# Optimization experiments

Measured on AMD Instinct MI355X. Metric: run time of the kernel, lower is better.

## Reference

```python
import jax, jax.numpy as jnp
import numpy as np

INPUT_DIM = 1024
OUTPUT_DIM = 1024


def setup_inputs() -> dict:
    key = jax.random.key(0)
    k1, k2, k3, k4 = jax.random.split(key, 4)
    B, S, D = 4, 2048, INPUT_DIM
    src = jax.random.normal(k1, (B, S, D), dtype=jnp.float32)
    tgt = jax.random.normal(k2, (B, S, D), dtype=jnp.float32)
    # nn.Linear(input_dim*2, output_dim): weight [out, in], bias [out]
    bound = 1.0 / np.sqrt(2 * D)
    W = jax.random.uniform(k3, (OUTPUT_DIM, 2 * D), jnp.float32, -bound, bound)
    b = jax.random.uniform(k4, (OUTPUT_DIM,), jnp.float32, -bound, bound)
    return {"src": src, "tgt": tgt, "W": W, "b": b}


def reference(src, tgt, W, b):
    # weight = bmm(tgt, src^T): [B, S_tgt, S_src]
    weight = jnp.einsum("btd,bsd->bts", tgt, src)
    # NOTE: original uses Softmax(dim=1) -> normalizes over the tgt axis
    weight = jax.nn.softmax(weight, axis=1)
    # weighted sum over src positions: [B, S_tgt, D]
    weight_sum = jnp.einsum("bts,bsd->btd", weight, src)
    output = jnp.concatenate([weight_sum, tgt], axis=2)  # [B, S_tgt, 2D]
    output = output @ W.T + b  # [B, S_tgt, output_dim]
    return (output, weight)
```

## Files before the change

kernel.cpp:

```cpp
#include <hip/hip_runtime.h>
#include <stdint.h>


#define B_   4
#define S_   2048
#define D_   1024
#define OUTD 1024

typedef unsigned short ushort_t;
typedef _Float16 half8 __attribute__((ext_vector_type(8)));
typedef float    f32x4 __attribute__((ext_vector_type(4)));

__device__ __forceinline__ ushort_t f2h(float f) {
    union { _Float16 h; ushort_t u; } v;
    v.h = (_Float16)f;
    return v.u;
}
__device__ __forceinline__ float h2f(ushort_t u) {
    union { _Float16 h; ushort_t u; } v;
    v.u = u;
    return (float)v.h;
}

__device__ __forceinline__ void ld16(const ushort_t* g, ushort_t* l) {
    __builtin_amdgcn_global_load_lds(
        (const __attribute__((address_space(1))) void*)g,
        (__attribute__((address_space(3))) void*)l, 16, 0, 0);
}


__global__ void k_split(const float4* __restrict__ src, const float4* __restrict__ tgt,
                        ushort4* __restrict__ sh,
                        ushort4* __restrict__ th, ushort4* __restrict__ tl)
{
    const int64_t n4 = (int64_t)B_ * S_ * D_ / 4;
    for (int64_t i = (int64_t)blockIdx.x * blockDim.x + threadIdx.x; i < n4;
         i += (int64_t)gridDim.x * blockDim.x) {
        float4 s = src[i];
        sh[i] = (ushort4){f2h(s.x), f2h(s.y), f2h(s.z), f2h(s.w)};
        float4 tv = tgt[i];
        ushort4 ht = {f2h(tv.x), f2h(tv.y), f2h(tv.z), f2h(tv.w)};
        th[i] = ht;
        tl[i] = (ushort4){f2h(tv.x - h2f(ht.x)), f2h(tv.y - h2f(ht.y)),
                          f2h(tv.z - h2f(ht.z)), f2h(tv.w - h2f(ht.w))};
    }
}

__global__ void k_wconv(const float4* __restrict__ W, ushort4* __restrict__ wb)
{
    const int64_t n4 = (int64_t)OUTD * 2 * D_ / 4;
    for (int64_t i = (int64_t)blockIdx.x * blockDim.x + threadIdx.x; i < n4;
         i += (int64_t)gridDim.x * blockDim.x) {
        float4 w = W[i];
        wb[i] = (ushort4){f2h(w.x), f2h(w.y), f2h(w.z), f2h(w.w)};
    }
}

__launch_bounds__(512, 2)
__global__ void k_gemm_logits(const ushort_t* __restrict__ Ah, const ushort_t* __restrict__ Al,
                              const ushort_t* __restrict__ Bs,
                              float* __restrict__ C,
                              float* __restrict__ pm, float* __restrict__ ps)
{
    const int M = S_, N = S_, K = D_;
    int b = blockIdx.z;
    Ah += (int64_t)b * M * K;  Al += (int64_t)b * M * K;
    Bs += (int64_t)b * N * K;
    C  += (int64_t)b * M * N;

    __shared__ __align__(16) ushort_t lds[2 * 24576];
    __shared__ float red_m[4][256], red_s[4][256];

    int t    = threadIdx.x;
    int m0   = blockIdx.y * 256, n0 = blockIdx.x * 256;
    int wave = t >> 6, lane = t & 63;
    int wr   = (wave >> 1) * 64;
    int wc   = (wave & 1) * 128;
    int l15  = lane & 15, quad = lane >> 4;

    f32x4 acc[4][8];
#pragma unroll
    for (int i = 0; i < 4; i++)
#pragma unroll
        for (int j = 0; j < 8; j++) acc[i][j] = (f32x4){0.f, 0.f, 0.f, 0.f};

    int pr   = t >> 3;
    int slot = t & 7;
    int cg   = slot ^ (pr & 7);
    int srow = pr * 2 + (cg >> 2);
    int scol = (cg & 3) * 8;

    const ushort_t* gAh = Ah + (int64_t)(m0 + srow) * K + scol;
    const ushort_t* gAl = Al + (int64_t)(m0 + srow) * K + scol;
    const ushort_t* gB  = Bs + (int64_t)(n0 + srow) * K + scol;
    const int64_t rstep = (int64_t)128 * K;

    auto stage = [&](int bufi, int kofs) {
        ushort_t* Lb = lds + bufi * 24576 + t * 8;
        ld16(gAh + kofs,         Lb);
        ld16(gAh + rstep + kofs, Lb + 4096);
        ld16(gAl + kofs,         Lb + 8192);
        ld16(gAl + rstep + kofs, Lb + 12288);
        ld16(gB  + kofs,         Lb + 16384);
        ld16(gB  + rstep + kofs, Lb + 20480);
    };

    int aoff[4], boff[8];
#pragma unroll
    for (int i = 0; i < 4; i++) {
        int R = wr + i * 16 + l15;
        int p = R >> 1, c = ((R & 1) << 2) + quad;
        aoff[i] = p * 64 + ((c ^ (p & 7)) << 3);
    }
#pragma unroll
    for (int j = 0; j < 8; j++) {
        int R = wc + j * 16 + l15;
        int p = R >> 1, c = ((R & 1) << 2) + quad;
        boff[j] = p * 64 + ((c ^ (p & 7)) << 3);
    }

    stage(0, 0);
    int buf = 0;

    for (int kt = 0; kt < 32; ++kt) {
        asm volatile("s_waitcnt vmcnt(0)" ::: "memory");
        __builtin_amdgcn_s_barrier();
        asm volatile("" ::: "memory");
        __builtin_amdgcn_sched_barrier(0);

        if (kt < 31) stage(buf ^ 1, (kt + 1) * 32);

        const ushort_t* Lb = lds + buf * 24576;
        half8 ah[4], al[4], bf[4];
#pragma unroll
        for (int i = 0; i < 4; i++) {
            ah[i] = *(const half8*)(Lb + aoff[i]);
            al[i] = *(const half8*)(Lb + 8192 + aoff[i]);
        }
#pragma unroll
        for (int j = 0; j < 4; j++) bf[j] = *(const half8*)(Lb + 16384 + boff[j]);

        __builtin_amdgcn_s_setprio(1);
#pragma unroll
        for (int i = 0; i < 4; i++)
#pragma unroll
            for (int j = 0; j < 4; j++)
                acc[i][j] = __builtin_amdgcn_mfma_f32_16x16x32_f16(ah[i], bf[j], acc[i][j], 0, 0, 0);
#pragma unroll
        for (int i = 0; i < 4; i++)
#pragma unroll
            for (int j = 0; j < 4; j++)
                acc[i][j] = __builtin_amdgcn_mfma_f32_16x16x32_f16(al[i], bf[j], acc[i][j], 0, 0, 0);
        __builtin_amdgcn_s_setprio(0);

#pragma unroll
        for (int j = 0; j < 4; j++) bf[j] = *(const half8*)(Lb + 16384 + boff[4 + j]);

        __builtin_amdgcn_s_setprio(1);
#pragma unroll
        for (int i = 0; i < 4; i++)
#pragma unroll
            for (int j = 0; j < 4; j++)
                acc[i][4 + j] = __builtin_amdgcn_mfma_f32_16x16x32_f16(ah[i], bf[j], acc[i][4 + j], 0, 0, 0);
#pragma unroll
        for (int i = 0; i < 4; i++)
#pragma unroll
            for (int j = 0; j < 4; j++)
                acc[i][4 + j] = __builtin_amdgcn_mfma_f32_16x16x32_f16(al[i], bf[j], acc[i][4 + j], 0, 0, 0);
        __builtin_amdgcn_s_setprio(0);

        buf ^= 1;
    }

#pragma unroll
    for (int i = 0; i < 4; i++) {
        int row_base = m0 + wr + i * 16 + quad * 4;
#pragma unroll
        for (int j = 0; j < 8; j++) {
            int col = n0 + wc + j * 16 + l15;
#pragma unroll
            for (int r = 0; r < 4; r++)
                C[(int64_t)(row_base + r) * N + col] = acc[i][j][r];
        }
    }

    int wrow = wave >> 1;
#pragma unroll
    for (int j = 0; j < 8; j++) {
        float m = -3.0e38f;
#pragma unroll
        for (int i = 0; i < 4; i++)
#pragma unroll
            for (int r = 0; r < 4; r++) m = fmaxf(m, acc[i][j][r]);
        float s = 0.f;
#pragma unroll
        for (int i = 0; i < 4; i++)
#pragma unroll
            for (int r = 0; r < 4; r++) s += __expf(acc[i][j][r] - m);
#pragma unroll
        for (int d = 16; d <= 32; d <<= 1) {
            float m2 = __shfl_xor(m, d, 64);
            float s2 = __shfl_xor(s, d, 64);
            float nm = fmaxf(m, m2);
            s = s * __expf(m - nm) + s2 * __expf(m2 - nm);
            m = nm;
        }
        if (lane < 16) {
            red_m[wrow][wc + j * 16 + l15] = m;
            red_s[wrow][wc + j * 16 + l15] = s;
        }
    }
    __syncthreads();
    if (t < 256) {
        float m = red_m[0][t];
#pragma unroll
        for (int w = 1; w < 4; w++) m = fmaxf(m, red_m[w][t]);
        float s = 0.f;
#pragma unroll
        for (int w = 0; w < 4; w++) s += red_s[w][t] * __expf(red_m[w][t] - m);
        int idx = blockIdx.y * (B_ * S_) + b * S_ + n0 + t;
        pm[idx] = m;
        ps[idx] = s;
    }
}


__global__ void k_colstats2(const float* __restrict__ pm, const float* __restrict__ ps,
                            float* __restrict__ cmax, float* __restrict__ cinv)
{
    int i = blockIdx.x * 256 + threadIdx.x;
    float m = -3.0e38f;
#pragma unroll
    for (int c = 0; c < 8; c++) m = fmaxf(m, pm[c * (B_ * S_) + i]);
    float sum = 0.f;
#pragma unroll
    for (int c = 0; c < 8; c++) sum += ps[c * (B_ * S_) + i] * __expf(pm[c * (B_ * S_) + i] - m);
    cmax[i] = m;
    cinv[i] = 1.0f / sum;
}

__global__ void k_softmax_norm(float4* __restrict__ L, const float4* __restrict__ cmax4,
                               const float4* __restrict__ cinv4, ushort4* __restrict__ wbf)
{
    const int64_t n4 = (int64_t)B_ * S_ * S_ / 4;
    for (int64_t i = (int64_t)blockIdx.x * blockDim.x + threadIdx.x; i < n4;
         i += (int64_t)gridDim.x * blockDim.x) {
        int b  = (int)(i >> 20);
        int c4 = (int)(i & 511);
        float4 x  = L[i];
        float4 cm = cmax4[b * 512 + c4];
        float4 ci = cinv4[b * 512 + c4];
        float4 w;
        w.x = __expf(x.x - cm.x) * ci.x;
        w.y = __expf(x.y - cm.y) * ci.y;
        w.z = __expf(x.z - cm.z) * ci.z;
        w.w = __expf(x.w - cm.w) * ci.w;
        L[i] = w;
        wbf[i] = (ushort4){f2h(w.x), f2h(w.y), f2h(w.z), f2h(w.w)};
    }
}

__launch_bounds__(512, 2)
__global__ void k_gemm_nt2(const ushort_t* __restrict__ A, int lda, int64_t bsA,
                           const ushort_t* __restrict__ Bm, int ldb, int64_t bsB,
                           ushort_t* __restrict__ C, int ldc, int64_t bsC, int K)
{
    int b = blockIdx.z;
    A  += (int64_t)b * bsA;
    Bm += (int64_t)b * bsB;
    C  += (int64_t)b * bsC;

    __shared__ __align__(16) ushort_t lds[2 * 24576];

    int t    = threadIdx.x;
    int m0   = blockIdx.y * 256, n0 = blockIdx.x * 128;
    int wave = t >> 6, lane = t & 63;
    int wr   = (wave >> 1) * 64;
    int wc   = (wave & 1) * 64;
    int l15  = lane & 15, quad = lane >> 4;

    f32x4 acc[4][4];
#pragma unroll
    for (int i = 0; i < 4; i++)
#pragma unroll
        for (int j = 0; j < 4; j++) acc[i][j] = (f32x4){0.f, 0.f, 0.f, 0.f};

    int srow = t >> 3;
    int cg   = (t & 7) ^ (srow & 7);
    int scol = cg * 8;

    const ushort_t* gA = A  + (int64_t)(m0 + srow) * lda + scol;
    const ushort_t* gB = Bm + (int64_t)(n0 + srow) * ldb + scol;

    auto stage = [&](int bufi, int k0) {
        ushort_t* Lb = lds + bufi * 24576 + t * 8;
        ld16(gA + k0,                        Lb);
        ld16(gA + (int64_t)64  * lda + k0,   Lb + 4096);
        ld16(gA + (int64_t)128 * lda + k0,   Lb + 8192);
        ld16(gA + (int64_t)192 * lda + k0,   Lb + 12288);
        ld16(gB + k0,                        Lb + 16384);
        ld16(gB + (int64_t)64  * ldb + k0,   Lb + 20480);
    };

    int aoff[4][2], boff[4][2];
#pragma unroll
    for (int i = 0; i < 4; i++) {
        int R = wr + i * 16 + l15;
#pragma unroll
        for (int h = 0; h < 2; h++) {
            int c = quad + h * 4;
            aoff[i][h] = R * 64 + ((c ^ (R & 7)) << 3);
        }
    }
#pragma unroll
    for (int j = 0; j < 4; j++) {
        int R = wc + j * 16 + l15;
#pragma unroll
        for (int h = 0; h < 2; h++) {
            int c = quad + h * 4;
            boff[j][h] = 16384 + R * 64 + ((c ^ (R & 7)) << 3);
        }
    }

    stage(0, 0);
    int buf = 0;
    const int NT = K >> 6;

    for (int kt = 0; kt < NT; ++kt) {
        asm volatile("s_waitcnt vmcnt(0)" ::: "memory");
        __builtin_amdgcn_s_barrier();
        asm volatile("" ::: "memory");
        __builtin_amdgcn_sched_barrier(0);

        if (kt + 1 < NT) stage(buf ^ 1, (kt + 1) * 64);

        const ushort_t* Lb = lds + buf * 24576;
#pragma unroll
        for (int h = 0; h < 2; h++) {
            half8 af[4], bf[4];
#pragma unroll
            for (int i = 0; i < 4; i++) af[i] = *(const half8*)(Lb + aoff[i][h]);
#pragma unroll
            for (int j = 0; j < 4; j++) bf[j] = *(const half8*)(Lb + boff[j][h]);
            __builtin_amdgcn_s_setprio(1);
#pragma unroll
            for (int i = 0; i < 4; i++)
#pragma unroll
                for (int j = 0; j < 4; j++)
                    acc[i][j] = __builtin_amdgcn_mfma_f32_16x16x32_f16(af[i], bf[j], acc[i][j], 0, 0, 0);
            __builtin_amdgcn_s_setprio(0);
        }
        buf ^= 1;
    }

#pragma unroll
    for (int i = 0; i < 4; i++) {
        int row_base = m0 + wr + i * 16 + quad * 4;
#pragma unroll
        for (int j = 0; j < 4; j++) {
            int col = n0 + wc + j * 16 + l15;
#pragma unroll
            for (int r = 0; r < 4; r++)
                C[(int64_t)(row_base + r) * ldc + col] = f2h(acc[i][j][r]);
        }
    }
}

__launch_bounds__(512, 2)
__global__ void k_gemm_final(const ushort_t* __restrict__ Wt, const ushort_t* __restrict__ PT,
                             const ushort_t* __restrict__ Q, const float* __restrict__ bias,
                             float* __restrict__ out)
{
    const int K = S_, N = OUTD;
    int b = blockIdx.z;
    const ushort_t* A  = Wt + (int64_t)b * S_ * S_;
    const ushort_t* Bm = PT + (int64_t)b * OUTD * S_;
    const ushort_t* Qb = Q  + (int64_t)b * S_ * OUTD;
    float* Cb = out + (int64_t)b * S_ * OUTD;

    __shared__ __align__(16) ushort_t lds[2 * 24576];

    int t    = threadIdx.x;
    int m0   = blockIdx.y * 256, n0 = blockIdx.x * 128;
    int wave = t >> 6, lane = t & 63;
    int wr   = (wave >> 1) * 64;
    int wc   = (wave & 1) * 64;
    int l15  = lane & 15, quad = lane >> 4;

    f32x4 acc[4][4];
#pragma unroll
    for (int i = 0; i < 4; i++)
#pragma unroll
        for (int j = 0; j < 4; j++) acc[i][j] = (f32x4){0.f, 0.f, 0.f, 0.f};

    int srow = t >> 3;
    int cg   = (t & 7) ^ (srow & 7);
    int scol = cg * 8;

    const ushort_t* gA = A  + (int64_t)(m0 + srow) * K + scol;
    const ushort_t* gB = Bm + (int64_t)(n0 + srow) * K + scol;

    auto stage = [&](int bufi, int k0) {
        ushort_t* Lb = lds + bufi * 24576 + t * 8;
        ld16(gA + k0,                      Lb);
        ld16(gA + (int64_t)64  * K + k0,   Lb + 4096);
        ld16(gA + (int64_t)128 * K + k0,   Lb + 8192);
        ld16(gA + (int64_t)192 * K + k0,   Lb + 12288);
        ld16(gB + k0,                      Lb + 16384);
        ld16(gB + (int64_t)64  * K + k0,   Lb + 20480);
    };

    int aoff[4][2], boff[4][2];
#pragma unroll
    for (int i = 0; i < 4; i++) {
        int R = wr + i * 16 + l15;
#pragma unroll
        for (int h = 0; h < 2; h++) {
            int c = quad + h * 4;
            aoff[i][h] = R * 64 + ((c ^ (R & 7)) << 3);
        }
    }
#pragma unroll
    for (int j = 0; j < 4; j++) {
        int R = wc + j * 16 + l15;
#pragma unroll
        for (int h = 0; h < 2; h++) {
            int c = quad + h * 4;
            boff[j][h] = 16384 + R * 64 + ((c ^ (R & 7)) << 3);
        }
    }

    stage(0, 0);
    int buf = 0;
    const int NT = K >> 6;

    for (int kt = 0; kt < NT; ++kt) {
        asm volatile("s_waitcnt vmcnt(0)" ::: "memory");
        __builtin_amdgcn_s_barrier();
        asm volatile("" ::: "memory");
        __builtin_amdgcn_sched_barrier(0);

        if (kt + 1 < NT) stage(buf ^ 1, (kt + 1) * 64);

        const ushort_t* Lb = lds + buf * 24576;
#pragma unroll
        for (int h = 0; h < 2; h++) {
            half8 af[4], bf[4];
#pragma unroll
            for (int i = 0; i < 4; i++) af[i] = *(const half8*)(Lb + aoff[i][h]);
#pragma unroll
            for (int j = 0; j < 4; j++) bf[j] = *(const half8*)(Lb + boff[j][h]);
            __builtin_amdgcn_s_setprio(1);
#pragma unroll
            for (int i = 0; i < 4; i++)
#pragma unroll
                for (int j = 0; j < 4; j++)
                    acc[i][j] = __builtin_amdgcn_mfma_f32_16x16x32_f16(af[i], bf[j], acc[i][j], 0, 0, 0);
            __builtin_amdgcn_s_setprio(0);
        }
        buf ^= 1;
    }

#pragma unroll
    for (int i = 0; i < 4; i++) {
        int row_base = m0 + wr + i * 16 + quad * 4;
#pragma unroll
        for (int j = 0; j < 4; j++) {
            int col = n0 + wc + j * 16 + l15;
            float bv = bias[col];
#pragma unroll
            for (int r = 0; r < 4; r++) {
                int64_t idx = (int64_t)(row_base + r) * N + col;
                Cb[idx] = acc[i][j][r] + h2f(Qb[idx]) + bv;
            }
        }
    }
}


extern "C" void kernel_launch(void* const* d_in, const int* in_sizes, int n_in,
                              void* d_out, int out_size, void* d_ws, size_t ws_size,
                              hipStream_t stream)
{
    const float* src  = (const float*)d_in[0];
    const float* tgt  = (const float*)d_in[1];
    const float* W    = (const float*)d_in[2];
    const float* bias = (const float*)d_in[3];

    float* out = (float*)d_out;
    float* Lw  = out + (size_t)B_ * S_ * OUTD;

    char*  ws = (char*)d_ws;
    size_t o  = 0;
    auto take = [&](size_t bytes) -> char* {
        char* p = ws + o;
        o += (bytes + 255) & ~(size_t)255;
        return p;
    };
    const size_t ELEMS = (size_t)B_ * S_ * D_;
    ushort_t* sh   = (ushort_t*)take(ELEMS * 2);
    ushort_t* th   = (ushort_t*)take(ELEMS * 2);
    ushort_t* tl   = (ushort_t*)take(ELEMS * 2);
    ushort_t* wbf  = (ushort_t*)take((size_t)B_ * S_ * S_ * 2);
    ushort_t* wb   = (ushort_t*)take((size_t)OUTD * 2 * D_ * 2);
    ushort_t* PT   = (ushort_t*)take((size_t)B_ * OUTD * S_ * 2);
    ushort_t* Qb   = (ushort_t*)take((size_t)B_ * S_ * OUTD * 2);
    float*    pm   = (float*)take(16 * (size_t)B_ * S_ * 4);
    float*    ps   = (float*)take(16 * (size_t)B_ * S_ * 4);
    float*    cmax = (float*)take((size_t)B_ * S_ * 4);
    float*    cinv = (float*)take((size_t)B_ * S_ * 4);
    (void)ws_size; (void)in_sizes; (void)n_in; (void)out_size;

    k_split<<<dim3(2048), dim3(256), 0, stream>>>((const float4*)src, (const float4*)tgt,
                                                  (ushort4*)sh, (ushort4*)th, (ushort4*)tl);
    k_wconv<<<dim3(512), dim3(256), 0, stream>>>((const float4*)W, (ushort4*)wb);

    k_gemm_nt2<<<dim3(16, 4, 4), dim3(512), 0, stream>>>(
        wb, 2 * D_, 0,
        sh, D_, (int64_t)S_ * D_,
        PT, S_, (int64_t)OUTD * S_, D_);

    k_gemm_nt2<<<dim3(8, 8, 4), dim3(512), 0, stream>>>(
        th, D_, (int64_t)S_ * D_,
        wb + D_, 2 * D_, 0,
        Qb, OUTD, (int64_t)S_ * OUTD, D_);

    k_gemm_logits<<<dim3(8, 8, 4), dim3(512), 0, stream>>>(th, tl, sh, Lw, pm, ps);

    k_colstats2<<<dim3(32), dim3(256), 0, stream>>>(pm, ps, cmax, cinv);
    k_softmax_norm<<<dim3(2048), dim3(256), 0, stream>>>((float4*)Lw, (const float4*)cmax,
                                                         (const float4*)cinv, (ushort4*)wbf);

    k_gemm_final<<<dim3(8, 8, 4), dim3(512), 0, stream>>>(wbf, PT, Qb, bias, out);
}
```

Measured before the change: 347.7 us.

## Triple-buffer LDS staging in all three GEMM kernels with two-deep prefetch

Moves the logits, nt2 and final GEMM kernels from double to triple shared-memory buffering. Two K-tiles are prefetched ahead, and the wait is relaxed to vmcnt(6) so the tile after the current one can stay in flight. The aim is to hide more global-load latency behind the MFMA work. The cost is that LDS per block grows to about 144 KB (more in the logits kernel), which likely stops two 512-thread blocks from sharing a CU and so reduces occupancy.

```diff
diff --git a/kernel.cpp b/kernel.cpp
--- a/kernel.cpp
+++ b/kernel.cpp
@@ -68,7 +68,7 @@
     Bs += (int64_t)b * N * K;
     C  += (int64_t)b * M * N;
 
-    __shared__ __align__(16) ushort_t lds[2 * 24576];
+    __shared__ __align__(16) ushort_t lds[3 * 24576];
     __shared__ float red_m[4][256], red_s[4][256];
 
     int t    = threadIdx.x;
@@ -120,17 +120,22 @@
     }
 
     stage(0, 0);
-    int buf = 0;
-
-    for (int kt = 0; kt < 32; ++kt) {
-        asm volatile("s_waitcnt vmcnt(0)" ::: "memory");
+    stage(1, 32);
+    const int NT = 32;
+
+    for (int kt = 0; kt < NT; ++kt) {
+        if (kt + 1 < NT) {
+            asm volatile("s_waitcnt vmcnt(6)" ::: "memory");
+        } else {
+            asm volatile("s_waitcnt vmcnt(0)" ::: "memory");
+        }
         __builtin_amdgcn_s_barrier();
         asm volatile("" ::: "memory");
         __builtin_amdgcn_sched_barrier(0);
 
-        if (kt < 31) stage(buf ^ 1, (kt + 1) * 32);
-
-        const ushort_t* Lb = lds + buf * 24576;
+        if (kt + 2 < NT) stage((kt + 2) % 3, (kt + 2) * 32);
+
+        const ushort_t* Lb = lds + (kt % 3) * 24576;
         half8 ah[4], al[4], bf[4];
 #pragma unroll
         for (int i = 0; i < 4; i++) {
@@ -168,8 +173,6 @@
             for (int j = 0; j < 4; j++)
                 acc[i][4 + j] = __builtin_amdgcn_mfma_f32_16x16x32_f16(al[i], bf[j], acc[i][4 + j], 0, 0, 0);
         __builtin_amdgcn_s_setprio(0);
-
-        buf ^= 1;
     }
 
 #pragma unroll
@@ -270,7 +273,7 @@
     Bm += (int64_t)b * bsB;
     C  += (int64_t)b * bsC;
 
-    __shared__ __align__(16) ushort_t lds[2 * 24576];
+    __shared__ __align__(16) ushort_t lds[3 * 24576];
 
     int t    = threadIdx.x;
     int m0   = blockIdx.y * 256, n0 = blockIdx.x * 128;
@@ -322,19 +325,23 @@
         }
     }
 
+    const int NT = K >> 6;
     stage(0, 0);
-    int buf = 0;
-    const int NT = K >> 6;
+    stage(1, 64);
 
     for (int kt = 0; kt < NT; ++kt) {
-        asm volatile("s_waitcnt vmcnt(0)" ::: "memory");
+        if (kt + 1 < NT) {
+            asm volatile("s_waitcnt vmcnt(6)" ::: "memory");
+        } else {
+            asm volatile("s_waitcnt vmcnt(0)" ::: "memory");
+        }
         __builtin_amdgcn_s_barrier();
         asm volatile("" ::: "memory");
         __builtin_amdgcn_sched_barrier(0);
 
-        if (kt + 1 < NT) stage(buf ^ 1, (kt + 1) * 64);
-
-        const ushort_t* Lb = lds + buf * 24576;
+        if (kt + 2 < NT) stage((kt + 2) % 3, (kt + 2) * 64);
+
+        const ushort_t* Lb = lds + (kt % 3) * 24576;
 #pragma unroll
         for (int h = 0; h < 2; h++) {
             half8 af[4], bf[4];
@@ -350,7 +357,6 @@
                     acc[i][j] = __builtin_amdgcn_mfma_f32_16x16x32_f16(af[i], bf[j], acc[i][j], 0, 0, 0);
             __builtin_amdgcn_s_setprio(0);
         }
-        buf ^= 1;
     }
 
 #pragma unroll
@@ -378,7 +384,7 @@
     const ushort_t* Qb = Q  + (int64_t)b * S_ * OUTD;
     float* Cb = out + (int64_t)b * S_ * OUTD;
 
-    __shared__ __align__(16) ushort_t lds[2 * 24576];
+    __shared__ __align__(16) ushort_t lds[3 * 24576];
 
     int t    = threadIdx.x;
     int m0   = blockIdx.y * 256, n0 = blockIdx.x * 128;
@@ -430,19 +436,23 @@
         }
     }
 
+    const int NT = K >> 6;
     stage(0, 0);
-    int buf = 0;
-    const int NT = K >> 6;
+    stage(1, 64);
 
     for (int kt = 0; kt < NT; ++kt) {
-        asm volatile("s_waitcnt vmcnt(0)" ::: "memory");
+        if (kt + 1 < NT) {
+            asm volatile("s_waitcnt vmcnt(6)" ::: "memory");
+        } else {
+            asm volatile("s_waitcnt vmcnt(0)" ::: "memory");
+        }
         __builtin_amdgcn_s_barrier();
         asm volatile("" ::: "memory");
         __builtin_amdgcn_sched_barrier(0);
 
-        if (kt + 1 < NT) stage(buf ^ 1, (kt + 1) * 64);
-
-        const ushort_t* Lb = lds + buf * 24576;
+        if (kt + 2 < NT) stage((kt + 2) % 3, (kt + 2) * 64);
+
+        const ushort_t* Lb = lds + (kt % 3) * 24576;
 #pragma unroll
         for (int h = 0; h < 2; h++) {
             half8 af[4], bf[4];
@@ -458,7 +468,6 @@
                     acc[i][j] = __builtin_amdgcn_mfma_f32_16x16x32_f16(af[i], bf[j], acc[i][j], 0, 0, 0);
             __builtin_amdgcn_s_setprio(0);
         }
-        buf ^= 1;
     }
 
 #pragma unroll
```

Result: no change. 351.7 us (+1.2%).
